# Optimization experiments

Hardware: AMD Instinct MI355X
Metric: run time of the kernel (lower is better)

Reference implementation:

```python
import jax, jax.numpy as jnp
import numpy as np
import math

B, S, HID, H = 4, 4096, 1024, 16
DH = HID // H  # 64

def setup_inputs() -> dict:
    key = jax.random.key(0)
    ks = jax.random.split(key, 6)
    query = jax.random.normal(ks[0], (B, S, HID), dtype=jnp.float32)
    key_t = jax.random.normal(ks[1], (B, S, HID), dtype=jnp.float32)
    value = jax.random.normal(ks[2], (B, S, HID), dtype=jnp.float32)
    attn_mask = jax.random.normal(ks[3], (B, S, H, H), dtype=jnp.float32)
    # nn.Linear(hidden, 3*hidden): weight (3H, H), bias (3H,)
    W_qkv = jax.random.normal(ks[4], (3 * HID, HID), dtype=jnp.float32) * (1.0 / math.sqrt(HID))
    b_qkv = jax.random.normal(ks[5], (3 * HID,), dtype=jnp.float32) * 0.01
    return {"query": query, "key": key_t, "value": value, "attn_mask": attn_mask,
            "W_qkv": W_qkv, "b_qkv": b_qkv}

def reference(query, key, value, attn_mask, W_qkv, b_qkv):
    # fused QKV projection (only `query` is used, matching the source)
    qkv = jnp.einsum('bsh,oh->bso', query, W_qkv) + b_qkv  # (B,S,3*HID)
    q, k, v = jnp.split(qkv, 3, axis=-1)
    q = q.reshape(B, S, H, DH)
    k = k.reshape(B, S, H, DH)
    v = v.reshape(B, S, H, DH)
    # NOTE: no (B,H,S,D) permute in the source -> scores are head-vs-head per position
    scale = 1.0 / math.sqrt(DH)
    qk = jnp.einsum('bshd,bsgd->bshg', q, k) * scale + attn_mask  # (B,S,H,H)
    attn_weight = jax.nn.softmax(qk, axis=-1)
    # dropout_p=0 (eval): identity
    o = jnp.einsum('bshg,bsgd->bshd', attn_weight, v)  # (B,S,H,DH)
    return o.reshape(B, S, HID)
```

## Files before the change

### kernel.cpp

```cpp
#include <hip/hip_runtime.h>
#include <cstdint>
#include <cstddef>


typedef __attribute__((ext_vector_type(8))) short bf16x8;
typedef __attribute__((ext_vector_type(4))) float f32x4;

__device__ inline unsigned short f2bf(float f) {
  unsigned int i = __float_as_uint(f);
  i += 0x7fff + ((i >> 16) & 1);
  return (unsigned short)(i >> 16);
}

__device__ inline void async16(const void* g, void* l) {
  __builtin_amdgcn_global_load_lds(
      (const __attribute__((address_space(1))) void*)g,
      (__attribute__((address_space(3))) void*)l, 16, 0, 0);
}

__device__ inline void unpack8(bf16x8 v, float* f) {
  union { bf16x8 s; unsigned int u[4]; } x; x.s = v;
  #pragma unroll
  for (int i = 0; i < 4; ++i) {
    f[2 * i]     = __uint_as_float(x.u[i] << 16);
    f[2 * i + 1] = __uint_as_float(x.u[i] & 0xffff0000u);
  }
}

__global__ __launch_bounds__(256) void cast_kernel(const float* __restrict__ in,
                                                   unsigned short* __restrict__ out,
                                                   int n) {
  int i = (blockIdx.x * 256 + threadIdx.x) * 4;
  if (i >= n) return;
  float4 v = *(const float4*)(in + i);
  union { unsigned short u[4]; unsigned long long ll; } o;
  o.u[0] = f2bf(v.x); o.u[1] = f2bf(v.y); o.u[2] = f2bf(v.z); o.u[3] = f2bf(v.w);
  *(unsigned long long*)(out + i) = o.ll;
}

#define GK 1024
#define GN 3072
__global__ __launch_bounds__(512, 2) void gemm_qkv(const unsigned short* __restrict__ A,
                                                   const unsigned short* __restrict__ Bm,
                                                   const float* __restrict__ bias,
                                                   unsigned short* __restrict__ C) {
  __shared__ unsigned short As[2][256][64];
  __shared__ unsigned short Bs[2][256][64];

  const int bid = blockIdx.x;
  const int swz = (bid & 7) * 96 + (bid >> 3);
  const int m0 = (swz / 12) * 256;
  const int n0 = (swz % 12) * 256;

  const int tid  = threadIdx.x;
  const int lane = tid & 63;
  const int wave = tid >> 6;
  const int wm = wave & 1;
  const int wn = wave >> 1;
  const int fr = lane & 15;
  const int fq = lane >> 4;

  const int r0 = tid >> 3;
  const int c0 = (tid & 7) ^ (r0 & 7);
  const unsigned short* gA = A  + (size_t)(m0 + r0) * GK + c0 * 8;
  const unsigned short* gB = Bm + (size_t)(n0 + r0) * GK + c0 * 8;
  const int ls0 = wave * 512;

#define STAGE_A(tt, hh) do {                                                   \
    unsigned short* lb_ = &As[(tt) & 1][(hh) * 128][0];                        \
    const unsigned short* g_ = gA + (size_t)(hh) * 128 * GK + (tt) * 64;       \
    async16(g_, lb_ + ls0);                                                    \
    async16(g_ + (size_t)64 * GK, lb_ + 4096 + ls0);                           \
  } while (0)
#define STAGE_B(tt, hh) do {                                                   \
    unsigned short* lb_ = &Bs[(tt) & 1][(hh) * 128][0];                        \
    const unsigned short* g_ = gB + (size_t)(hh) * 128 * GK + (tt) * 64;       \
    async16(g_, lb_ + ls0);                                                    \
    async16(g_ + (size_t)64 * GK, lb_ + 4096 + ls0);                           \
  } while (0)

#define READ_A4(bp, ph) do {                                                   \
    _Pragma("unroll")                                                          \
    for (int ii = 0; ii < 2; ++ii) {                                           \
      const int rA = ((ph) * 2 + ii) * 32 + wm * 16 + fr;                      \
      _Pragma("unroll")                                                        \
      for (int ks = 0; ks < 2; ++ks)                                           \
        af[ii][ks] = *(const bf16x8*)&As[bp][rA][((ks * 4 + fq) ^ (rA & 7)) * 8]; \
    } } while (0)

#define READ_B8(bp) do {                                                       \
    _Pragma("unroll")                                                          \
    for (int j = 0; j < 4; ++j) {                                              \
      const int rB = wn * 64 + j * 16 + fr;                                    \
      _Pragma("unroll")                                                        \
      for (int ks = 0; ks < 2; ++ks)                                           \
        bfr[j][ks] = *(const bf16x8*)&Bs[bp][rB][((ks * 4 + fq) ^ (rB & 7)) * 8]; \
    } } while (0)

#define MFMA_PHASE(ph) do {                                                    \
    __builtin_amdgcn_s_setprio(1);                                             \
    _Pragma("unroll")                                                          \
    for (int ks = 0; ks < 2; ++ks)                                             \
      _Pragma("unroll")                                                        \
      for (int ii = 0; ii < 2; ++ii)                                           \
        _Pragma("unroll")                                                      \
        for (int j = 0; j < 4; ++j)                                            \
          acc[(ph) * 2 + ii][j] = __builtin_amdgcn_mfma_f32_16x16x32_bf16(     \
              af[ii][ks], bfr[j][ks], acc[(ph) * 2 + ii][j], 0, 0, 0);         \
    __builtin_amdgcn_s_setprio(0);                                             \
  } while (0)

  f32x4 acc[8][4] = {};
  bf16x8 af[2][2];
  bf16x8 bfr[4][2];

  STAGE_A(0, 0); STAGE_A(0, 1); STAGE_B(0, 0); STAGE_B(0, 1);
  STAGE_A(1, 0); STAGE_A(1, 1); STAGE_B(1, 0); STAGE_B(1, 1);
  asm volatile("s_waitcnt vmcnt(8)\n\ts_barrier" ::: "memory");
  __builtin_amdgcn_sched_barrier(0);
  READ_A4(0, 0);
  READ_B8(0);

  for (int t = 0; t < 16; ++t) {
    const int cur = t & 1, nxt = cur ^ 1;
    asm volatile("s_waitcnt lgkmcnt(0)\n\ts_barrier" ::: "memory");
    __builtin_amdgcn_sched_barrier(0);
    MFMA_PHASE(0);
    READ_A4(cur, 1);
    asm volatile("s_waitcnt lgkmcnt(0)\n\ts_barrier" ::: "memory");
    __builtin_amdgcn_sched_barrier(0);
    MFMA_PHASE(1);
    READ_A4(cur, 2);
    asm volatile("s_waitcnt vmcnt(0) lgkmcnt(0)\n\ts_barrier" ::: "memory");
    __builtin_amdgcn_sched_barrier(0);
    MFMA_PHASE(2);
    READ_A4(cur, 3);
    if (t + 2 < 16) { STAGE_B(t + 2, 0); }
    asm volatile("s_waitcnt lgkmcnt(0)\n\ts_barrier" ::: "memory");
    __builtin_amdgcn_sched_barrier(0);
    MFMA_PHASE(3);
    if (t + 1 < 16) { READ_A4(nxt, 0); READ_B8(nxt); }
    if (t + 2 < 16) { STAGE_A(t + 2, 0); STAGE_A(t + 2, 1); STAGE_B(t + 2, 1); }
  }
#undef STAGE_A
#undef STAGE_B
#undef READ_A4
#undef READ_B8
#undef MFMA_PHASE

  #pragma unroll
  for (int i = 0; i < 8; ++i) {
    #pragma unroll
    for (int j = 0; j < 4; ++j) {
      const int col = n0 + wn * 64 + j * 16 + fr;
      const float bc = bias[col];
      const int rowb = m0 + i * 32 + wm * 16 + fq * 4;
      #pragma unroll
      for (int rr = 0; rr < 4; ++rr)
        C[(size_t)(rowb + rr) * GN + col] = f2bf(acc[i][j][rr] + bc);
    }
  }
}

__global__ __launch_bounds__(256) void attn_kernel(const unsigned short* __restrict__ QKV,
                                                   const float* __restrict__ mask,
                                                   float* __restrict__ out) {
  __shared__ unsigned short shKV[4][2048];
  const int wave = threadIdx.x >> 6;
  const int lane = threadIdx.x & 63;
  const int pos = blockIdx.x * 4 + wave;

  const unsigned short* row = QKV + (size_t)pos * 3072;

  #pragma unroll
  for (int t = 0; t < 4; ++t)
    async16(&row[1024 + t * 512 + (size_t)lane * 8], &shKV[wave][t * 512]);

  bf16x8 q0 = *(const bf16x8*)&row[lane * 16];
  bf16x8 q1 = *(const bf16x8*)&row[lane * 16 + 8];

  const int h = lane >> 2;
  const int dg = lane & 3;

  const float* mrow = mask + (size_t)pos * 256 + h * 16;
  float4 m4[4];
  #pragma unroll
  for (int t = 0; t < 4; ++t) m4[t] = *(const float4*)&mrow[t * 4];

  float q[16];
  unpack8(q0, q);
  unpack8(q1, q + 8);

  asm volatile("s_waitcnt vmcnt(0)" ::: "memory");

  float s[16];
  #pragma unroll
  for (int g = 0; g < 16; ++g) {
    const unsigned short* kp = &shKV[wave][g * 64 + dg * 16];
    float kf[16];
    unpack8(*(const bf16x8*)kp, kf);
    unpack8(*(const bf16x8*)(kp + 8), kf + 8);
    float acc = 0.f;
    #pragma unroll
    for (int d = 0; d < 16; ++d) acc += q[d] * kf[d];
    s[g] = acc;
  }
  #pragma unroll
  for (int g = 0; g < 16; ++g) {
    s[g] += __shfl_xor(s[g], 1);
    s[g] += __shfl_xor(s[g], 2);
  }

  const float* mp = (const float*)m4;
  float mx = -1e30f;
  #pragma unroll
  for (int g = 0; g < 16; ++g) {
    s[g] = s[g] * 0.125f + mp[g];
    mx = fmaxf(mx, s[g]);
  }
  float sum = 0.f;
  #pragma unroll
  for (int g = 0; g < 16; ++g) { s[g] = __expf(s[g] - mx); sum += s[g]; }
  float inv = 1.f / sum;

  float o[16];
  #pragma unroll
  for (int dd = 0; dd < 16; ++dd) o[dd] = 0.f;
  #pragma unroll
  for (int g = 0; g < 16; ++g) {
    const unsigned short* vp = &shKV[wave][1024 + g * 64 + dg * 16];
    float vf[16];
    unpack8(*(const bf16x8*)vp, vf);
    unpack8(*(const bf16x8*)(vp + 8), vf + 8);
    float p = s[g];
    #pragma unroll
    for (int dd = 0; dd < 16; ++dd) o[dd] += p * vf[dd];
  }

  float* op = out + (size_t)pos * 1024 + lane * 16;
  #pragma unroll
  for (int t = 0; t < 4; ++t) {
    float4 w;
    w.x = o[t * 4 + 0] * inv; w.y = o[t * 4 + 1] * inv;
    w.z = o[t * 4 + 2] * inv; w.w = o[t * 4 + 3] * inv;
    *(float4*)(op + t * 4) = w;
  }
}

extern "C" void kernel_launch(void* const* d_in, const int* in_sizes, int n_in,
                              void* d_out, int out_size, void* d_ws, size_t ws_size,
                              hipStream_t stream) {
  const float* query = (const float*)d_in[0];
  const float* mask  = (const float*)d_in[3];
  const float* Wqkv  = (const float*)d_in[4];
  const float* bqkv  = (const float*)d_in[5];
  float* out = (float*)d_out;

  unsigned short* qb   = (unsigned short*)d_ws;
  unsigned short* wb   = (unsigned short*)((char*)d_ws + 33554432);
  unsigned short* qkvb = (unsigned short*)((char*)d_ws + 39845888);

  cast_kernel<<<16384, 256, 0, stream>>>(query, qb, 16777216);
  cast_kernel<<<3072, 256, 0, stream>>>(Wqkv, wb, 3145728);

  gemm_qkv<<<768, 512, 0, stream>>>(qb, wb, bqkv, qkvb);

  attn_kernel<<<4096, 256, 0, stream>>>(qkvb, mask, out);
}
```

Baseline: 340.5 us.

## Replace hand-scheduled GEMM pipeline with single-barrier one-ahead prefetch loop

Drops the two-tile-ahead prefetch with four fine-grained waitcnt/barrier phases per K-step in the QKV projection GEMM. It uses one __syncthreads per iteration, issues the async LDS loads for the next tile, and then runs all MFMAs on the current tile. Two A-fragment register sets alternate so that LDS reads for the next phase can overlap the MFMAs of the current one. This cuts the number of barriers and the scheduling constraints, but global-load latency is now hidden by only one tile of lookahead and the register pressure rises.

```diff
diff --git a/kernel.cpp b/kernel.cpp
--- a/kernel.cpp
+++ b/kernel.cpp
@@ -79,13 +79,13 @@
     async16(g_ + (size_t)64 * GK, lb_ + 4096 + ls0);                           \
   } while (0)
 
-#define READ_A4(bp, ph) do {                                                   \
+#define READ_A4(AF, bp, ph) do {                                               \
     _Pragma("unroll")                                                          \
     for (int ii = 0; ii < 2; ++ii) {                                           \
       const int rA = ((ph) * 2 + ii) * 32 + wm * 16 + fr;                      \
       _Pragma("unroll")                                                        \
       for (int ks = 0; ks < 2; ++ks)                                           \
-        af[ii][ks] = *(const bf16x8*)&As[bp][rA][((ks * 4 + fq) ^ (rA & 7)) * 8]; \
+        AF[ii][ks] = *(const bf16x8*)&As[bp][rA][((ks * 4 + fq) ^ (rA & 7)) * 8]; \
     } } while (0)
 
 #define READ_B8(bp) do {                                                       \
@@ -97,7 +97,7 @@
         bfr[j][ks] = *(const bf16x8*)&Bs[bp][rB][((ks * 4 + fq) ^ (rB & 7)) * 8]; \
     } } while (0)
 
-#define MFMA_PHASE(ph) do {                                                    \
+#define MFMA16(ph, AF) do {                                                    \
     __builtin_amdgcn_s_setprio(1);                                             \
     _Pragma("unroll")                                                          \
     for (int ks = 0; ks < 2; ++ks)                                             \
@@ -106,47 +106,37 @@
         _Pragma("unroll")                                                      \
         for (int j = 0; j < 4; ++j)                                            \
           acc[(ph) * 2 + ii][j] = __builtin_amdgcn_mfma_f32_16x16x32_bf16(     \
-              af[ii][ks], bfr[j][ks], acc[(ph) * 2 + ii][j], 0, 0, 0);         \
+              AF[ii][ks], bfr[j][ks], acc[(ph) * 2 + ii][j], 0, 0, 0);         \
     __builtin_amdgcn_s_setprio(0);                                             \
   } while (0)
 
   f32x4 acc[8][4] = {};
-  bf16x8 af[2][2];
+  bf16x8 af0[2][2], af1[2][2];
   bf16x8 bfr[4][2];
 
   STAGE_A(0, 0); STAGE_A(0, 1); STAGE_B(0, 0); STAGE_B(0, 1);
-  STAGE_A(1, 0); STAGE_A(1, 1); STAGE_B(1, 0); STAGE_B(1, 1);
-  asm volatile("s_waitcnt vmcnt(8)\n\ts_barrier" ::: "memory");
-  __builtin_amdgcn_sched_barrier(0);
-  READ_A4(0, 0);
-  READ_B8(0);
 
   for (int t = 0; t < 16; ++t) {
-    const int cur = t & 1, nxt = cur ^ 1;
-    asm volatile("s_waitcnt lgkmcnt(0)\n\ts_barrier" ::: "memory");
-    __builtin_amdgcn_sched_barrier(0);
-    MFMA_PHASE(0);
-    READ_A4(cur, 1);
-    asm volatile("s_waitcnt lgkmcnt(0)\n\ts_barrier" ::: "memory");
-    __builtin_amdgcn_sched_barrier(0);
-    MFMA_PHASE(1);
-    READ_A4(cur, 2);
-    asm volatile("s_waitcnt vmcnt(0) lgkmcnt(0)\n\ts_barrier" ::: "memory");
-    __builtin_amdgcn_sched_barrier(0);
-    MFMA_PHASE(2);
-    READ_A4(cur, 3);
-    if (t + 2 < 16) { STAGE_B(t + 2, 0); }
-    asm volatile("s_waitcnt lgkmcnt(0)\n\ts_barrier" ::: "memory");
-    __builtin_amdgcn_sched_barrier(0);
-    MFMA_PHASE(3);
-    if (t + 1 < 16) { READ_A4(nxt, 0); READ_B8(nxt); }
-    if (t + 2 < 16) { STAGE_A(t + 2, 0); STAGE_A(t + 2, 1); STAGE_B(t + 2, 1); }
+    const int cur = t & 1;
+    __syncthreads();
+    if (t + 1 < 16) {
+      STAGE_A(t + 1, 0); STAGE_A(t + 1, 1); STAGE_B(t + 1, 0); STAGE_B(t + 1, 1);
+    }
+    READ_B8(cur);
+    READ_A4(af0, cur, 0);
+    READ_A4(af1, cur, 1);
+    MFMA16(0, af0);
+    READ_A4(af0, cur, 2);
+    MFMA16(1, af1);
+    READ_A4(af1, cur, 3);
+    MFMA16(2, af0);
+    MFMA16(3, af1);
   }
 #undef STAGE_A
 #undef STAGE_B
 #undef READ_A4
 #undef READ_B8
-#undef MFMA_PHASE
+#undef MFMA16
 
   #pragma unroll
   for (int i = 0; i < 8; ++i) {
```

Measured after the change: 342.7 us. Within noise of the previous version (+0.6%).
